# Kernel tuning notes

Measured on AMD Instinct MI355X. Metric: run time of the kernel, lower is better.

## Reference

```python
import jax, jax.numpy as jnp
import numpy as np

B, L, D, H = 2, 2048, 1024, 16
HD = D // H  # head_dim = 64


def setup_inputs() -> dict:
    key = jax.random.key(0)
    k1, k2, k3, k4, k5 = jax.random.split(key, 5)
    s = 1.0 / np.sqrt(D)
    return {
        "x": jax.random.normal(k1, (B, L, D), dtype=jnp.float32),
        "quantum_scores": jax.random.normal(k2, (B, L, L), dtype=jnp.float32),
        "wq": jax.random.normal(k3, (D, D), dtype=jnp.float32) * s,
        "wk": jax.random.normal(k4, (D, D), dtype=jnp.float32) * s,
        "wv": jax.random.normal(k5, (D, D), dtype=jnp.float32) * s,
        "scale": jnp.ones((H, 1, 1), dtype=jnp.float32),
    }


def reference(x, quantum_scores, wq, wk, wv, scale):
    Bq, Lq, _ = x.shape
    # nn.Linear: y = x @ W^T ; then split heads -> (B, H, L, HD)
    def split_heads(t):
        return t.reshape(Bq, Lq, H, HD).transpose(0, 2, 1, 3)

    q = split_heads(x @ wq.T)
    k = split_heads(x @ wk.T)
    v = split_heads(x @ wv.T)

    logits = jnp.einsum("bhqd,bhkd->bhqk", q, k) / np.sqrt(HD).astype(np.float32)
    logits = logits + quantum_scores[:, None, :, :]          # quantum bias, broadcast over heads
    logits = logits * scale[None, :, :, :]                   # per-head learnable scale
    attn = jax.nn.softmax(logits, axis=-1)
    out = jnp.einsum("bhqk,bhkd->bhqd", attn, v)
    return out.transpose(0, 2, 1, 3).reshape(Bq, Lq, D)
```

## Files before the change

### kernel.cpp

```cpp
#include <hip/hip_runtime.h>

#define Bq 2
#define Lq 2048
#define Dq 1024
#define Hq 16
#define HDq 64

typedef _Float16 f16;
typedef _Float16 f16x8 __attribute__((ext_vector_type(8)));
typedef _Float16 f16x4 __attribute__((ext_vector_type(4)));
typedef __fp16 hf16x2 __attribute__((ext_vector_type(2)));
typedef float f32x4 __attribute__((ext_vector_type(4)));
typedef float f32x16 __attribute__((ext_vector_type(16)));

__device__ __forceinline__ void gload_lds16(const void* g, void* l) {
    __builtin_amdgcn_global_load_lds(
        (const __attribute__((address_space(1))) unsigned int*)g,
        (__attribute__((address_space(3))) unsigned int*)l, 16, 0, 0);
}

__device__ __forceinline__ void swap32(int& a, int& b) {
    asm volatile("v_permlane32_swap_b32 %0, %1" : "+v"(a), "+v"(b));
}

__device__ __forceinline__ int pk2(float a, float b) {
    hf16x2 v = __builtin_amdgcn_cvt_pkrtz(a, b);
    return __builtin_bit_cast(int, v);
}

__global__ __launch_bounds__(256) void convert_kernel(
    const float* __restrict__ x,
    const float* __restrict__ wq, const float* __restrict__ wk, const float* __restrict__ wv,
    f16* __restrict__ x_h, f16* __restrict__ wq_h, f16* __restrict__ wk_h, f16* __restrict__ wv_h)
{
    const int NX = Bq*Lq*Dq;
    const int NW = Dq*Dq;
    const int total4 = (NX + 3*NW) / 4;
    for (int i = blockIdx.x*blockDim.x + threadIdx.x; i < total4;
         i += gridDim.x*blockDim.x) {
        int e = i * 4;
        const float* src; f16* dst; int off;
        if (e < NX) { src = x; dst = x_h; off = e; }
        else {
            int t = e - NX; int w = t >> 20; off = t & (NW-1);
            src = (w==0) ? wq : (w==1) ? wk : wv;
            dst = (w==0) ? wq_h : (w==1) ? wk_h : wv_h;
        }
        float4 v = *reinterpret_cast<const float4*>(src + off);
        f16x4 hv; hv.x=(f16)v.x; hv.y=(f16)v.y; hv.z=(f16)v.z; hv.w=(f16)v.w;
        *reinterpret_cast<f16x4*>(dst + off) = hv;
    }
}

#define GBM 128
#define GBN 128
#define GBK 32

__global__ __launch_bounds__(256) void qkv_mfma_kernel(
    const f16* __restrict__ x_h,
    const f16* __restrict__ wq_h, const f16* __restrict__ wk_h, const f16* __restrict__ wv_h,
    f16* __restrict__ q_h, f16* __restrict__ k_h, f16* __restrict__ vT_h)
{
    __shared__ __align__(16) f16 As[GBM*GBK];
    __shared__ __align__(16) f16 Bs[GBN*GBK];

    const int tid  = threadIdx.x;
    const int lane = tid & 63;
    const int wave = tid >> 6;
    const int wr = wave >> 1, wc = wave & 1;
    const int l15 = lane & 15, l4 = lane >> 4;
    const int n0 = blockIdx.x * GBN;
    const int m0 = blockIdx.y * GBM;
    const int z  = blockIdx.z;
    const f16* W = (z==0) ? wq_h : (z==1) ? wk_h : wv_h;

    const int sslot = tid & 3;

    f32x4 acc[4][4];
    #pragma unroll
    for (int i=0;i<4;++i)
        #pragma unroll
        for (int j=0;j<4;++j) acc[i][j] = f32x4{0.f,0.f,0.f,0.f};

    for (int kt = 0; kt < Dq; kt += GBK) {
        __syncthreads();
        #pragma unroll
        for (int j = 0; j < 2; ++j) {
            int slotIdx = tid + j*256;
            int row = slotIdx >> 2;
            gload_lds16(x_h + (size_t)(m0+row)*Dq + kt + sslot*8,
                        (char*)As + slotIdx*16);
            gload_lds16(W   + (size_t)(n0+row)*Dq + kt + sslot*8,
                        (char*)Bs + slotIdx*16);
        }
        __syncthreads();

        f16x8 a[4], b[4];
        #pragma unroll
        for (int m=0;m<4;++m) {
            int row = wr*64 + m*16 + l15;
            a[m] = *reinterpret_cast<const f16x8*>((const char*)As + row*64 + l4*16);
        }
        #pragma unroll
        for (int n=0;n<4;++n) {
            int row = wc*64 + n*16 + l15;
            b[n] = *reinterpret_cast<const f16x8*>((const char*)Bs + row*64 + l4*16);
        }
        #pragma unroll
        for (int m=0;m<4;++m)
            #pragma unroll
            for (int n=0;n<4;++n)
                acc[m][n] = __builtin_amdgcn_mfma_f32_16x16x32_f16(a[m], b[n], acc[m][n], 0,0,0);
    }

    #pragma unroll
    for (int m=0;m<4;++m) {
        #pragma unroll
        for (int r=0;r<4;++r) {
            int grow = m0 + wr*64 + m*16 + l4*4 + r;
            int b_   = grow >> 11;
            int lrow = grow & (Lq-1);
            #pragma unroll
            for (int n=0;n<4;++n) {
                int gcol = n0 + wc*64 + n*16 + l15;
                int h = gcol >> 6, d = gcol & 63;
                int bh = b_*Hq + h;
                f16 val = (f16)acc[m][n][r];
                if (z==0)      q_h[((size_t)bh*Lq + lrow)*HDq + d] = val;
                else if (z==1) k_h[((size_t)bh*Lq + lrow)*HDq + d] = val;
                else           vT_h[((size_t)bh*HDq + d)*Lq + lrow] = val;
            }
        }
    }
}

__global__ __launch_bounds__(256) void qm_pre_kernel(
    const float* __restrict__ quantum, f16* __restrict__ qm_pre)
{
    __shared__ float qs[32][64];
    const int tid = threadIdx.x;
    const int qt = blockIdx.x, kt = blockIdx.y, b = blockIdx.z;
    const float* base = quantum + ((size_t)b*Lq + qt*32)*Lq + kt*64;
    #pragma unroll
    for (int i=0;i<2;++i) {
        int idx = tid + i*256;
        int r = idx >> 4, c = (idx & 15)*4;
        float4 v = *reinterpret_cast<const float4*>(base + (size_t)r*Lq + c);
        qs[r][c]=v.x; qs[r][c+1]=v.y; qs[r][c+2]=v.z; qs[r][c+3]=v.w;
    }
    __syncthreads();
    const int seg = tid >> 6, lane = tid & 63, l31 = lane & 31, hi = lane >> 5;
    f16x8 u;
    #pragma unroll
    for (int e=0;e<8;++e) {
        int key = 16*seg + 8*(e>>2) + 4*hi + (e&3);
        u[e] = (f16)qs[l31][key];
    }
    f16* outp = qm_pre + (((size_t)b*32 + kt)*64 + qt)*2048 + seg*512 + lane*8;
    *reinterpret_cast<f16x8*>(outp) = u;
}

__global__ __launch_bounds__(512, 2) void attn8_kernel(
    const f16* __restrict__ q_h, const f16* __restrict__ k_h, const f16* __restrict__ vT_h,
    const f16* __restrict__ qm_pre, const float* __restrict__ scale,
    float* __restrict__ out)
{
    __shared__ __align__(16) char lds[32768];

    const int tid  = threadIdx.x;
    const int lane = tid & 63;
    const int wave = tid >> 6;
    const int l31  = lane & 31;
    const int hi   = lane >> 5;
    const int bh = blockIdx.x;
    const int qb = blockIdx.y;
    const int b_ = bh >> 4, h = bh & 15;
    const int qW = qb*256 + wave*32;
    const int qt = qb*8 + wave;
    const float sc = scale[h];
    const float c1 = 0.125f * sc * 1.44269504f;
    const float c2 = sc * 1.44269504f;

    const f16* kbase = k_h  + (size_t)bh*Lq*HDq;
    const f16* vbase = vT_h + (size_t)bh*HDq*Lq;

    f16x8 qf[4];
    {
        const f16* qb_ = q_h + ((size_t)bh*Lq + qW + l31)*HDq + hi*8;
        #pragma unroll
        for (int ds=0; ds<4; ++ds)
            qf[ds] = *reinterpret_cast<const f16x8*>(qb_ + ds*16);
    }

    f32x16 o0, o1;
    #pragma unroll
    for (int r=0;r<16;++r) { o0[r]=0.f; o1[r]=0.f; }
    float m_run = -1e30f, s_run = 0.f;

    auto STAGE = [&](int t, int buf) {
        const int k0 = t*64;
        char* LK = lds + buf*16384;
        char* LV = LK + 8192;
        int row = tid >> 3, slot = tid & 7;
        int ss = slot ^ (row & 7);
        gload_lds16(kbase + (size_t)(k0+row)*HDq + ss*8, LK + tid*16);
        gload_lds16(vbase + (size_t)row*Lq + k0 + ss*8,  LV + tid*16);
    };

    auto COMPUTE = [&](int t, int buf) {
        const char* LK = lds + buf*16384;
        const char* LV = LK + 8192;
        f16x8 qm[4];
        const f16* qmb = qm_pre + (((size_t)b_*32 + t)*64 + qt)*2048 + lane*8;
        #pragma unroll
        for (int s=0;s<4;++s)
            qm[s] = *reinterpret_cast<const f16x8*>(qmb + s*512);

        f32x16 st[2];
        __builtin_amdgcn_s_setprio(1);
        #pragma unroll
        for (int kt=0;kt<2;++kt) {
            #pragma unroll
            for (int r=0;r<16;++r) st[kt][r]=0.f;
            #pragma unroll
            for (int ds=0;ds<4;++ds) {
                f16x8 ka = *reinterpret_cast<const f16x8*>(
                    LK + ((kt*32+l31)<<7) + (((ds*2+hi)^(l31&7))<<4));
                st[kt] = __builtin_amdgcn_mfma_f32_32x32x16_f16(ka, qf[ds], st[kt], 0,0,0);
            }
        }
        __builtin_amdgcn_s_setprio(0);

        float lg[32];
        #pragma unroll
        for (int s=0;s<4;++s)
            #pragma unroll
            for (int e=0;e<8;++e) {
                int i = s*8 + e;
                float sv = (i < 16) ? st[0][i] : st[1][i-16];
                lg[i] = sv*c1 + (float)qm[s][e]*c2;
            }

        float tm[16];
        #pragma unroll
        for (int r=0;r<16;++r) tm[r] = fmaxf(lg[r], lg[r+16]);
        #pragma unroll
        for (int w=8; w>0; w>>=1)
            #pragma unroll
            for (int r=0;r<w;++r) tm[r] = fmaxf(tm[r], tm[r+w]);
        float tmax = fmaxf(tm[0], __shfl_xor(tm[0], 32));

        if (!__all(tmax <= m_run + 8.f)) {
            float m_new = fmaxf(m_run, tmax);
            float corr = __builtin_amdgcn_exp2f(m_run - m_new);
            m_run = m_new;
            s_run *= corr;
            #pragma unroll
            for (int r=0;r<16;++r) { o0[r] *= corr; o1[r] *= corr; }
        }

        float p[32];
        #pragma unroll
        for (int r=0;r<32;++r) p[r] = __builtin_amdgcn_exp2f(lg[r] - m_run);
        float sm[16];
        #pragma unroll
        for (int r=0;r<16;++r) sm[r] = p[r] + p[r+16];
        #pragma unroll
        for (int w=8; w>0; w>>=1)
            #pragma unroll
            for (int r=0;r<w;++r) sm[r] += sm[r+w];
        s_run += sm[0];

        f16x8 pb[4];
        #pragma unroll
        for (int ks=0; ks<4; ++ks) {
            int w0 = pk2(p[8*ks+0], p[8*ks+1]);
            int w1 = pk2(p[8*ks+2], p[8*ks+3]);
            int w2 = pk2(p[8*ks+4], p[8*ks+5]);
            int w3 = pk2(p[8*ks+6], p[8*ks+7]);
            swap32(w0, w2);
            swap32(w1, w3);
            union { int w[4]; f16x8 v; } u;
            u.w[0]=w0; u.w[1]=w1; u.w[2]=w2; u.w[3]=w3;
            pb[ks] = u.v;
        }

        __builtin_amdgcn_s_setprio(1);
        #pragma unroll
        for (int ks=0; ks<4; ++ks) {
            f16x8 va0 = *reinterpret_cast<const f16x8*>(
                LV + (l31<<7)        + (((ks*2+hi)^(l31&7))<<4));
            f16x8 va1 = *reinterpret_cast<const f16x8*>(
                LV + ((32+l31)<<7)   + (((ks*2+hi)^(l31&7))<<4));
            o0 = __builtin_amdgcn_mfma_f32_32x32x16_f16(va0, pb[ks], o0, 0,0,0);
            o1 = __builtin_amdgcn_mfma_f32_32x32x16_f16(va1, pb[ks], o1, 0,0,0);
        }
        __builtin_amdgcn_s_setprio(0);
    };

    STAGE(0, 0);
    STAGE(1, 1);
    for (int t = 0; t < 31; ++t) {
        asm volatile("s_waitcnt vmcnt(2)" ::: "memory");
        __builtin_amdgcn_s_barrier();
        COMPUTE(t, t & 1);
        asm volatile("s_waitcnt lgkmcnt(0)" ::: "memory");
        __builtin_amdgcn_sched_barrier(0);
        __builtin_amdgcn_s_barrier();
        if (t < 30) STAGE(t+2, t & 1);
    }
    asm volatile("s_waitcnt vmcnt(0)" ::: "memory");
    __builtin_amdgcn_s_barrier();
    COMPUTE(31, 1);

    float s_tot = s_run + __shfl_xor(s_run, 32);
    float inv = 1.0f / s_tot;
    float* ob = out + ((size_t)b_*Lq + qW + l31)*Dq + h*HDq;
    #pragma unroll
    for (int r=0;r<16;++r) {
        int drow = (r&3) + 8*(r>>2) + 4*hi;
        ob[drow]      = o0[r]*inv;
        ob[32 + drow] = o1[r]*inv;
    }
}

extern "C" void kernel_launch(void* const* d_in, const int* in_sizes, int n_in,
                              void* d_out, int out_size, void* d_ws, size_t ws_size,
                              hipStream_t stream) {
    const float* x       = (const float*)d_in[0];
    const float* quantum = (const float*)d_in[1];
    const float* wq      = (const float*)d_in[2];
    const float* wk      = (const float*)d_in[3];
    const float* wv      = (const float*)d_in[4];
    const float* scale   = (const float*)d_in[5];
    float* out = (float*)d_out;

    f16* ws     = (f16*)d_ws;
    f16* x_h    = ws;
    f16* wq_h   = ws + 4194304;
    f16* wk_h   = ws + 5242880;
    f16* wv_h   = ws + 6291456;
    f16* q_h    = ws + 7340032;
    f16* k_h    = ws + 11534336;
    f16* vT_h   = ws + 15728640;
    f16* qm_pre = ws + 19922944;

    convert_kernel<<<1024, 256, 0, stream>>>(x, wq, wk, wv, x_h, wq_h, wk_h, wv_h);

    dim3 gq(64, 32, 2);
    qm_pre_kernel<<<gq, 256, 0, stream>>>(quantum, qm_pre);

    dim3 g1(Dq/GBN, (Bq*Lq)/GBM, 3);
    qkv_mfma_kernel<<<g1, 256, 0, stream>>>(x_h, wq_h, wk_h, wv_h, q_h, k_h, vT_h);

    dim3 g2(Bq*Hq, Lq/256);
    attn8_kernel<<<g2, 512, 0, stream>>>(q_h, k_h, vT_h, qm_pre, scale, out);
}
```

Baseline: 137.7 us.

## Use 4-wave attention blocks with triple-buffered K/V and prefetched bias

Shrinks the attention block from 8 to 4 waves, covering 128 query rows each, which doubles the grid. K/V staging moves from a double buffer to a triple-buffered LDS ring with a deeper vmcnt-based pipeline, and staging now runs before compute instead of after a second barrier. The precomputed quantum-bias tile for the next step is loaded one iteration ahead into alternating registers. The aim is to hide global load latency and cut barrier stalls, at the cost of more LDS per block, more register pressure, and K/V being reloaded by twice as many blocks.

Measured after the change: 130.7 us (median of 2 runs). 5.1% less time.

```diff
diff --git a/kernel.cpp b/kernel.cpp
--- a/kernel.cpp
+++ b/kernel.cpp
@@ -160,12 +160,12 @@
     *reinterpret_cast<f16x8*>(outp) = u;
 }
 
-__global__ __launch_bounds__(512, 2) void attn8_kernel(
+__global__ __launch_bounds__(256, 2) void attn4_kernel(
     const f16* __restrict__ q_h, const f16* __restrict__ k_h, const f16* __restrict__ vT_h,
     const f16* __restrict__ qm_pre, const float* __restrict__ scale,
     float* __restrict__ out)
 {
-    __shared__ __align__(16) char lds[32768];
+    __shared__ __align__(16) char lds[49152];
 
     const int tid  = threadIdx.x;
     const int lane = tid & 63;
@@ -175,8 +175,8 @@
     const int bh = blockIdx.x;
     const int qb = blockIdx.y;
     const int b_ = bh >> 4, h = bh & 15;
-    const int qW = qb*256 + wave*32;
-    const int qt = qb*8 + wave;
+    const int qW = qb*128 + wave*32;
+    const int qt = qb*4 + wave;
     const float sc = scale[h];
     const float c1 = 0.125f * sc * 1.44269504f;
     const float c2 = sc * 1.44269504f;
@@ -201,20 +201,28 @@
         const int k0 = t*64;
         char* LK = lds + buf*16384;
         char* LV = LK + 8192;
-        int row = tid >> 3, slot = tid & 7;
-        int ss = slot ^ (row & 7);
-        gload_lds16(kbase + (size_t)(k0+row)*HDq + ss*8, LK + tid*16);
-        gload_lds16(vbase + (size_t)row*Lq + k0 + ss*8,  LV + tid*16);
+        #pragma unroll
+        for (int i=0;i<2;++i) {
+            int g = tid + i*256;
+            int row = g >> 3, slot = g & 7;
+            int ss = slot ^ (row & 7);
+            gload_lds16(kbase + (size_t)(k0+row)*HDq + ss*8, LK + g*16);
+            gload_lds16(vbase + (size_t)row*Lq + k0 + ss*8,  LV + g*16);
+        }
     };
 
-    auto COMPUTE = [&](int t, int buf) {
+    auto QMLOAD = [&](int t, f16x8 (&qm)[4]) {
+        const f16* qmb = qm_pre + (((size_t)b_*32 + t)*64 + qt)*2048 + lane*8;
+        #pragma unroll
+        for (int s=0;s<4;++s)
+            qm[s] = *reinterpret_cast<const f16x8*>(qmb + s*512);
+    };
+
+    auto COMPUTE = [&](int t, int buf, f16x8 (&qmc)[4], f16x8 (&qmn)[4]) {
         const char* LK = lds + buf*16384;
         const char* LV = LK + 8192;
-        f16x8 qm[4];
-        const f16* qmb = qm_pre + (((size_t)b_*32 + t)*64 + qt)*2048 + lane*8;
-        #pragma unroll
-        for (int s=0;s<4;++s)
-            qm[s] = *reinterpret_cast<const f16x8*>(qmb + s*512);
+        int tn = (t+1 < 32) ? t+1 : 31;
+        QMLOAD(tn, qmn);
 
         f32x16 st[2];
         __builtin_amdgcn_s_setprio(1);
@@ -238,7 +246,7 @@
             for (int e=0;e<8;++e) {
                 int i = s*8 + e;
                 float sv = (i < 16) ? st[0][i] : st[1][i-16];
-                lg[i] = sv*c1 + (float)qm[s][e]*c2;
+                lg[i] = sv*c1 + (float)qmc[s][e]*c2;
             }
 
         float tm[16];
@@ -298,20 +306,30 @@
         __builtin_amdgcn_s_setprio(0);
     };
 
+    f16x8 qmE[4], qmO[4];
+
+    QMLOAD(0, qmE);
     STAGE(0, 0);
     STAGE(1, 1);
-    for (int t = 0; t < 31; ++t) {
-        asm volatile("s_waitcnt vmcnt(2)" ::: "memory");
-        __builtin_amdgcn_s_barrier();
-        COMPUTE(t, t & 1);
-        asm volatile("s_waitcnt lgkmcnt(0)" ::: "memory");
-        __builtin_amdgcn_sched_barrier(0);
-        __builtin_amdgcn_s_barrier();
-        if (t < 30) STAGE(t+2, t & 1);
-    }
-    asm volatile("s_waitcnt vmcnt(0)" ::: "memory");
-    __builtin_amdgcn_s_barrier();
-    COMPUTE(31, 1);
+
+    #define VMW(n) asm volatile("s_waitcnt vmcnt(" #n ")" ::: "memory")
+
+    VMW(4);  __builtin_amdgcn_s_barrier();
+    STAGE(2, 2);  COMPUTE(0, 0, qmE, qmO);
+    VMW(8);  __builtin_amdgcn_s_barrier();
+    STAGE(3, 0);  COMPUTE(1, 1, qmO, qmE);
+    for (int t = 2; t < 30; t += 2) {
+        VMW(12); __builtin_amdgcn_s_barrier();
+        STAGE(t+2, (t+2)%3); COMPUTE(t, t%3, qmE, qmO);
+        VMW(12); __builtin_amdgcn_s_barrier();
+        STAGE(t+3, (t+3)%3); COMPUTE(t+1, (t+1)%3, qmO, qmE);
+    }
+    VMW(12); __builtin_amdgcn_s_barrier();
+    COMPUTE(30, 0, qmE, qmO);
+    VMW(8);  __builtin_amdgcn_s_barrier();
+    COMPUTE(31, 1, qmO, qmE);
+
+    #undef VMW
 
     float s_tot = s_run + __shfl_xor(s_run, 32);
     float inv = 1.0f / s_tot;
@@ -353,6 +371,6 @@
     dim3 g1(Dq/GBN, (Bq*Lq)/GBM, 3);
     qkv_mfma_kernel<<<g1, 256, 0, stream>>>(x_h, wq_h, wk_h, wv_h, q_h, k_h, vT_h);
 
-    dim3 g2(Bq*Hq, Lq/256);
-    attn8_kernel<<<g2, 512, 0, stream>>>(q_h, k_h, vT_h, qm_pre, scale, out);
-}
+    dim3 g2(Bq*Hq, Lq/128);
+    attn4_kernel<<<g2, 256, 0, stream>>>(q_h, k_h, vT_h, qm_pre, scale, out);
+}
```
